# Kernel tuning notes

Measured on AMD Instinct MI355X. Metric: run time of the kernel, lower is better.

Reference implementation:

```python
import jax, jax.numpy as jnp
import numpy as np

N, H, C, G = 50000, 16, 8, 128   # nodes, heads, per-head channels, graphs
F_IN, NUM_CLASSES = 128, 2
E = 800000
HC = H * C
NEG_SLOPE = 0.2
BN_EPS = 1e-5


def setup_inputs() -> dict:
    key = jax.random.key(0)
    ks = jax.random.split(key, 32)
    s = 0.1
    p = lambda k, shape: (jax.random.normal(k, shape, jnp.float32) * s)
    inp = {
        "x": jax.random.normal(ks[0], (N, F_IN), jnp.float32),
        "edge_index": jax.random.randint(ks[1], (2, E), 0, N, dtype=jnp.int32),
        "batch": jnp.sort(jax.random.randint(ks[2], (N,), 0, G, dtype=jnp.int32)),
        # GAT layer 1 (in=F_IN)
        "W1": p(ks[3], (F_IN, HC)), "b1": p(ks[4], (HC,)),
        "asrc1": p(ks[5], (H, C)), "adst1": p(ks[6], (H, C)),
        "g1": 1.0 + p(ks[7], (HC,)), "beta1": p(ks[8], (HC,)),
        # GAT layer 2 (in=HC)
        "W2": p(ks[9], (HC, HC)), "b2": p(ks[10], (HC,)),
        "asrc2": p(ks[11], (H, C)), "adst2": p(ks[12], (H, C)),
        "g2": 1.0 + p(ks[13], (HC,)), "beta2": p(ks[14], (HC,)),
        # GAT layer 3
        "W3": p(ks[15], (HC, HC)), "b3": p(ks[16], (HC,)),
        "asrc3": p(ks[17], (H, C)), "adst3": p(ks[18], (H, C)),
        "g3": 1.0 + p(ks[19], (HC,)), "beta3": p(ks[20], (HC,)),
        # final linear + bn4
        "Wl": p(ks[21], (2 * HC, NUM_CLASSES)), "bl": p(ks[22], (NUM_CLASSES,)),
        "g4": 1.0 + p(ks[23], (NUM_CLASSES,)), "beta4": p(ks[24], (NUM_CLASSES,)),
    }
    return inp


def _gat(x, src, dst, W, b, asrc, adst):
    # x: [N, F_in] -> h: [N, H, C]
    h = (x @ W).reshape(N, H, C)
    a_s = jnp.einsum("nhc,hc->nh", h, asrc)  # [N,H]
    a_d = jnp.einsum("nhc,hc->nh", h, adst)
    e = jax.nn.leaky_relu(a_s[src] + a_d[dst], NEG_SLOPE)  # [E',H]
    # per-destination softmax (every node has a self loop -> segments non-empty)
    e_max = jax.ops.segment_max(e, dst, num_segments=N)
    ex = jnp.exp(e - e_max[dst])
    denom = jax.ops.segment_sum(ex, dst, num_segments=N)
    alpha = ex / (denom[dst] + 1e-16)  # [E',H]
    out = jax.ops.segment_sum(h[src] * alpha[:, :, None], dst, num_segments=N)
    return out.reshape(N, HC) + b


def _bn(x, g, beta):
    mu = jnp.mean(x, axis=0)
    var = jnp.mean((x - mu) ** 2, axis=0)  # biased, training-mode BN
    return (x - mu) * jax.lax.rsqrt(var + BN_EPS) * g + beta


def reference(x, edge_index, batch,
              W1, b1, asrc1, adst1, g1, beta1,
              W2, b2, asrc2, adst2, g2, beta2,
              W3, b3, asrc3, adst3, g3, beta3,
              Wl, bl, g4, beta4):
    # add self loops once (add_self_loops=True in every GATConv)
    loop = jnp.arange(N, dtype=edge_index.dtype)
    src = jnp.concatenate([edge_index[0], loop])
    dst = jnp.concatenate([edge_index[1], loop])

    h = jax.nn.relu(_bn(_gat(x, src, dst, W1, b1, asrc1, adst1), g1, beta1))
    h = jax.nn.relu(_bn(_gat(h, src, dst, W2, b2, asrc2, adst2), g2, beta2))
    h = jax.nn.relu(_bn(_gat(h, src, dst, W3, b3, asrc3, adst3), g3, beta3))

    pooled_sum = jax.ops.segment_sum(h, batch, num_segments=G)        # [G,HC]
    cnt = jax.ops.segment_sum(jnp.ones((N,), h.dtype), batch, num_segments=G)
    pooled_mean = pooled_sum / jnp.maximum(cnt, 1.0)[:, None]
    z = jnp.concatenate([pooled_mean, pooled_sum], axis=1)            # [G,2*HC]
    z = z @ Wl + bl
    return _bn(z, g4, beta4)
```

## Files before the change

### kernel.cpp

```cpp
#include <hip/hip_runtime.h>

#define NN 50000
#define NHEADS 16
#define NGRAPH 128
#define NEDGE 800000
#define NEP (NEDGE + NN)

#define EPB 2048
#define NBLK 416
#define NBUK 391
#define CASTB 3125
#define WTB 192

typedef float4 f4;
typedef __attribute__((ext_vector_type(4))) float f32x4;
typedef __attribute__((ext_vector_type(8))) short s8;

__device__ inline unsigned short f2b(float f) {
  union { float f; unsigned u; } v; v.f = f;
  unsigned r = v.u + 0x7FFFu + ((v.u >> 16) & 1u);
  return (unsigned short)(r >> 16);
}
__device__ inline float b2f(unsigned u16) {
  union { unsigned u; float f; } v; v.u = u16 << 16;
  return v.f;
}
__device__ inline float blo(unsigned u) {
  union { unsigned u; float f; } v; v.u = u << 16;
  return v.f;
}
__device__ inline float bhi(unsigned u) {
  union { unsigned u; float f; } v; v.u = u & 0xffff0000u;
  return v.f;
}


__global__ __launch_bounds__(256) void k_bhist(const int* __restrict__ ei, int* __restrict__ cntmat) {
  __shared__ int hist[NBUK];
  int t = threadIdx.x, b = blockIdx.x;
  for (int k = t; k < NBUK; k += 256) hist[k] = 0;
  __syncthreads();
  int i0 = b * EPB;
  int i1 = i0 + EPB < NEP ? i0 + EPB : NEP;
  for (int i = i0 + t; i < i1; i += 256) {
    int d = (i < NEDGE) ? ei[NEDGE + i] : (i - NEDGE);
    atomicAdd(&hist[d >> 7], 1);
  }
  __syncthreads();
  for (int k = t; k < NBUK; k += 256) cntmat[b * NBUK + k] = hist[k];
}

__global__ __launch_bounds__(512) void k_bscan(int* __restrict__ cntmat, int* __restrict__ btotal) {
  __shared__ int buf[512];
  int t = threadIdx.x, k = blockIdx.x;
  int v = (t < NBLK) ? cntmat[t * NBUK + k] : 0;
  buf[t] = v;
  __syncthreads();
  for (int off = 1; off < 512; off <<= 1) {
    int y = (t >= off) ? buf[t - off] : 0;
    __syncthreads();
    buf[t] += y;
    __syncthreads();
  }
  if (t < NBLK) cntmat[t * NBUK + k] = buf[t] - v;
  if (t == 511) btotal[k] = buf[511];
}

__global__ __launch_bounds__(512) void k_bbase(const int* __restrict__ btotal, int* __restrict__ bbase) {
  __shared__ int buf[512];
  int t = threadIdx.x;
  int v = (t < NBUK) ? btotal[t] : 0;
  buf[t] = v;
  __syncthreads();
  for (int off = 1; off < 512; off <<= 1) {
    int y = (t >= off) ? buf[t - off] : 0;
    __syncthreads();
    buf[t] += y;
    __syncthreads();
  }
  if (t < NBUK) bbase[t] = buf[t] - v;
  if (t == 511) bbase[NBUK] = buf[511];
}

__global__ __launch_bounds__(256) void k_bscatter(const int* __restrict__ ei, const int* __restrict__ cntmat,
                                                  const int* __restrict__ bbase, unsigned* __restrict__ pairs) {
  __shared__ int cur[NBUK];
  int t = threadIdx.x, b = blockIdx.x;
  for (int k = t; k < NBUK; k += 256) cur[k] = bbase[k] + cntmat[b * NBUK + k];
  __syncthreads();
  int i0 = b * EPB;
  int i1 = i0 + EPB < NEP ? i0 + EPB : NEP;
  for (int i = i0 + t; i < i1; i += 256) {
    int s, d;
    if (i < NEDGE) { s = ei[i]; d = ei[NEDGE + i]; }
    else { s = d = i - NEDGE; }
    int pos = atomicAdd(&cur[d >> 7], 1);
    pairs[pos] = ((unsigned)(d & 127) << 16) | (unsigned)s;
  }
}

__global__ __launch_bounds__(256) void k_bfinal(const unsigned* __restrict__ pairs, const int* __restrict__ bbase,
                                                int* __restrict__ row_off, int* __restrict__ colp) {
  __shared__ int cnt[128];
  __shared__ int buf[128];
  __shared__ int cur[128];
  int t = threadIdx.x, k = blockIdx.x;
  int n0 = k << 7;
  if (t < 128) cnt[t] = 0;
  __syncthreads();
  int p0 = bbase[k], p1 = bbase[k + 1];
  for (int i = p0 + t; i < p1; i += 256) atomicAdd(&cnt[pairs[i] >> 16], 1);
  __syncthreads();
  if (t < 128) buf[t] = cnt[t];
  __syncthreads();
  for (int off = 1; off < 128; off <<= 1) {
    int y = (t < 128 && t >= off) ? buf[t - off] : 0;
    __syncthreads();
    if (t < 128) buf[t] += y;
    __syncthreads();
  }
  if (t < 128) {
    int excl = buf[t] - cnt[t];
    cur[t] = p0 + excl;
    if (n0 + t < NN) row_off[n0 + t] = p0 + excl;
  }
  if (k == NBUK - 1 && t == 0) row_off[NN] = p1;
  __syncthreads();
  for (int i = p0 + t; i < p1; i += 256) {
    unsigned r = pairs[i];
    int pos = atomicAdd(&cur[r >> 16], 1);
    colp[pos] = (int)(r & 0xffffu);
  }
}


__global__ __launch_bounds__(256) void k_prep(const float* __restrict__ X, unsigned short* __restrict__ Xb,
                                              const float* __restrict__ W0, const float* __restrict__ W1, const float* __restrict__ W2,
                                              unsigned short* __restrict__ T0, unsigned short* __restrict__ T1, unsigned short* __restrict__ T2,
                                              const int* __restrict__ batch, int* __restrict__ gstart) {
  int b = blockIdx.x, t = threadIdx.x;
  if (b < CASTB) {
    int i = b * 256 + t;
    const f4* X4 = (const f4*)X;
    f4 a = X4[2 * i], c = X4[2 * i + 1];
    uint4 o;
    o.x = (unsigned)f2b(a.x) | ((unsigned)f2b(a.y) << 16);
    o.y = (unsigned)f2b(a.z) | ((unsigned)f2b(a.w) << 16);
    o.z = (unsigned)f2b(c.x) | ((unsigned)f2b(c.y) << 16);
    o.w = (unsigned)f2b(c.z) | ((unsigned)f2b(c.w) << 16);
    ((uint4*)Xb)[i] = o;
  } else if (b < CASTB + WTB) {
    int idx = (b - CASTB) * 256 + t;
    int L = idx >> 14, r = idx & 16383;
    int n = r >> 7, kk = r & 127;
    const float* W = (L == 0) ? W0 : (L == 1) ? W1 : W2;
    unsigned short* T = (L == 0) ? T0 : (L == 1) ? T1 : T2;
    T[n * 128 + kk] = f2b(W[kk * 128 + n]);
  } else {
    int g = t;
    if (g > NGRAPH) return;
    int lo = 0, hi = NN;
    while (lo < hi) { int mid = (lo + hi) >> 1; if (batch[mid] < g) lo = mid + 1; else hi = mid; }
    gstart[g] = lo;
  }
}


template<int FUSE>
__global__ __launch_bounds__(256) void k_gemm_t(const unsigned short* __restrict__ A, const unsigned short* __restrict__ Wt,
                                                const float* __restrict__ sc, unsigned short* __restrict__ Hb) {
  int w = threadIdx.x >> 6, l = threadIdx.x & 63;
  int r0 = blockIdx.x * 128 + w * 32;
  int lr = l & 15, lg = l >> 4;
  f32x4 acc[2][8];
#pragma unroll
  for (int m = 0; m < 2; ++m)
#pragma unroll
    for (int n = 0; n < 8; ++n) acc[m][n] = (f32x4){0.f, 0.f, 0.f, 0.f};

#pragma unroll
  for (int ks = 0; ks < 4; ++ks) {
    int koff = ks * 32 + lg * 8;
    s8 a[2];
    if constexpr (FUSE) {
      f4 s0 = *(const f4*)(sc + koff),       s1 = *(const f4*)(sc + koff + 4);
      f4 h0 = *(const f4*)(sc + 128 + koff), h1 = *(const f4*)(sc + 128 + koff + 4);
#pragma unroll
      for (int m = 0; m < 2; ++m) {
        int row = r0 + m * 16 + lr;
        row = (row < NN) ? row : (NN - 1);
        uint4 raw = *(const uint4*)(A + (size_t)row * 128 + koff);
        float v0 = fmaxf(blo(raw.x) * s0.x + h0.x, 0.f);
        float v1 = fmaxf(bhi(raw.x) * s0.y + h0.y, 0.f);
        float v2 = fmaxf(blo(raw.y) * s0.z + h0.z, 0.f);
        float v3 = fmaxf(bhi(raw.y) * s0.w + h0.w, 0.f);
        float v4 = fmaxf(blo(raw.z) * s1.x + h1.x, 0.f);
        float v5 = fmaxf(bhi(raw.z) * s1.y + h1.y, 0.f);
        float v6 = fmaxf(blo(raw.w) * s1.z + h1.z, 0.f);
        float v7 = fmaxf(bhi(raw.w) * s1.w + h1.w, 0.f);
        union { s8 v; uint4 u; } pk;
        pk.u.x = (unsigned)f2b(v0) | ((unsigned)f2b(v1) << 16);
        pk.u.y = (unsigned)f2b(v2) | ((unsigned)f2b(v3) << 16);
        pk.u.z = (unsigned)f2b(v4) | ((unsigned)f2b(v5) << 16);
        pk.u.w = (unsigned)f2b(v6) | ((unsigned)f2b(v7) << 16);
        a[m] = pk.v;
      }
    } else {
#pragma unroll
      for (int m = 0; m < 2; ++m) {
        int row = r0 + m * 16 + lr;
        row = (row < NN) ? row : (NN - 1);
        a[m] = *(const s8*)(A + (size_t)row * 128 + koff);
      }
    }
    s8 b[8];
#pragma unroll
    for (int n = 0; n < 8; ++n)
      b[n] = *(const s8*)(Wt + (size_t)(n * 16 + lr) * 128 + koff);
#pragma unroll
    for (int m = 0; m < 2; ++m)
#pragma unroll
      for (int n = 0; n < 8; ++n)
        acc[m][n] = __builtin_amdgcn_mfma_f32_16x16x32_bf16(a[m], b[n], acc[m][n], 0, 0, 0);
  }

#pragma unroll
  for (int m = 0; m < 2; ++m) {
    int rowb = r0 + m * 16 + lg * 4;
#pragma unroll
    for (int n = 0; n < 8; ++n) {
      int colb = n * 16 + lr;
#pragma unroll
      for (int reg = 0; reg < 4; ++reg) {
        int row = rowb + reg;
        if (row < NN) Hb[(size_t)row * 128 + colb] = f2b(acc[m][n][reg]);
      }
    }
  }
}


__global__ __launch_bounds__(256) void k_coef(const unsigned short* __restrict__ Hb, const float* __restrict__ asrc,
                                              const float* __restrict__ adst, unsigned short* __restrict__ Asb, float* __restrict__ Ad) {
  int idx = blockIdx.x * 256 + threadIdx.x;
  if (idx >= NN * NHEADS) return;
  int n = idx >> 4, hd = idx & 15;
  uint4 hv = *(const uint4*)(Hb + (size_t)n * 128 + hd * 8);
  float h0 = blo(hv.x), h1 = bhi(hv.x);
  float h2 = blo(hv.y), h3 = bhi(hv.y);
  float h4 = blo(hv.z), h5 = bhi(hv.z);
  float h6 = blo(hv.w), h7 = bhi(hv.w);
  const f4* s4 = (const f4*)(asrc + hd * 8);
  const f4* d4 = (const f4*)(adst + hd * 8);
  f4 sa = s4[0], sb = s4[1], da = d4[0], db = d4[1];
  float as_v = h0 * sa.x + h1 * sa.y + h2 * sa.z + h3 * sa.w + h4 * sb.x + h5 * sb.y + h6 * sb.z + h7 * sb.w;
  float ad_v = h0 * da.x + h1 * da.y + h2 * da.z + h3 * da.w + h4 * db.x + h5 * db.y + h6 * db.z + h7 * db.w;
  Asb[idx] = f2b(as_v);
  Ad[idx] = ad_v;
}


__global__ __launch_bounds__(256, 4) void k_agg(const unsigned short* __restrict__ Hb, const unsigned short* __restrict__ Asb,
                                                const float* __restrict__ Ad,
                                                const int* __restrict__ row_off, const int* __restrict__ col,
                                                unsigned short* __restrict__ Vb) {
  int node = blockIdx.x * 8 + (threadIdx.x >> 5);
  int l = threadIdx.x & 31;
  int h = l & 15, par = l >> 4;
  int e0 = row_off[node], e1 = row_off[node + 1];
  float adh = Ad[node * 16 + h];
  float den = 0.f;
  float acc[8] = {0.f, 0.f, 0.f, 0.f, 0.f, 0.f, 0.f, 0.f};
  int j = e0 + par;
  for (; j + 14 < e1; j += 16) {
    int s[8];
#pragma unroll
    for (int q = 0; q < 8; ++q) s[q] = col[j + 2 * q];
    float a[8];
#pragma unroll
    for (int q = 0; q < 8; ++q) a[q] = b2f(Asb[s[q] * 16 + h]);
    uint4 p[8];
#pragma unroll
    for (int q = 0; q < 8; ++q) p[q] = *(const uint4*)(Hb + (size_t)s[q] * 128 + h * 8);
#pragma unroll
    for (int q = 0; q < 8; ++q) {
      float e = a[q] + adh;
      e = (e > 0.f) ? e : 0.2f * e;
      a[q] = __expf(e);
      den += a[q];
    }
#pragma unroll
    for (int q = 0; q < 8; ++q) {
      acc[0] += a[q] * blo(p[q].x); acc[1] += a[q] * bhi(p[q].x);
      acc[2] += a[q] * blo(p[q].y); acc[3] += a[q] * bhi(p[q].y);
      acc[4] += a[q] * blo(p[q].z); acc[5] += a[q] * bhi(p[q].z);
      acc[6] += a[q] * blo(p[q].w); acc[7] += a[q] * bhi(p[q].w);
    }
  }
  for (; j + 6 < e1; j += 8) {
    int s[4];
#pragma unroll
    for (int q = 0; q < 4; ++q) s[q] = col[j + 2 * q];
    float a[4];
#pragma unroll
    for (int q = 0; q < 4; ++q) a[q] = b2f(Asb[s[q] * 16 + h]);
    uint4 p[4];
#pragma unroll
    for (int q = 0; q < 4; ++q) p[q] = *(const uint4*)(Hb + (size_t)s[q] * 128 + h * 8);
#pragma unroll
    for (int q = 0; q < 4; ++q) {
      float e = a[q] + adh;
      e = (e > 0.f) ? e : 0.2f * e;
      a[q] = __expf(e);
      den += a[q];
    }
#pragma unroll
    for (int q = 0; q < 4; ++q) {
      acc[0] += a[q] * blo(p[q].x); acc[1] += a[q] * bhi(p[q].x);
      acc[2] += a[q] * blo(p[q].y); acc[3] += a[q] * bhi(p[q].y);
      acc[4] += a[q] * blo(p[q].z); acc[5] += a[q] * bhi(p[q].z);
      acc[6] += a[q] * blo(p[q].w); acc[7] += a[q] * bhi(p[q].w);
    }
  }
  for (; j < e1; j += 2) {
    int s0 = col[j];
    float a0 = b2f(Asb[s0 * 16 + h]) + adh;
    uint4 p0 = *(const uint4*)(Hb + (size_t)s0 * 128 + h * 8);
    a0 = (a0 > 0.f) ? a0 : 0.2f * a0;
    float x0 = __expf(a0);
    den += x0;
    acc[0] += x0 * blo(p0.x); acc[1] += x0 * bhi(p0.x);
    acc[2] += x0 * blo(p0.y); acc[3] += x0 * bhi(p0.y);
    acc[4] += x0 * blo(p0.z); acc[5] += x0 * bhi(p0.z);
    acc[6] += x0 * blo(p0.w); acc[7] += x0 * bhi(p0.w);
  }
  den += __shfl_xor(den, 16);
#pragma unroll
  for (int k = 0; k < 8; ++k) acc[k] += __shfl_xor(acc[k], 16);
  if (par == 0) {
    float inv = 1.f / (den + 1e-16f);
    uint4 o;
    o.x = (unsigned)f2b(acc[0] * inv) | ((unsigned)f2b(acc[1] * inv) << 16);
    o.y = (unsigned)f2b(acc[2] * inv) | ((unsigned)f2b(acc[3] * inv) << 16);
    o.z = (unsigned)f2b(acc[4] * inv) | ((unsigned)f2b(acc[5] * inv) << 16);
    o.w = (unsigned)f2b(acc[6] * inv) | ((unsigned)f2b(acc[7] * inv) << 16);
    *(uint4*)(Vb + (size_t)node * 128 + h * 8) = o;
  }
}


#define BN_CHUNK 391

__global__ __launch_bounds__(256) void k_bnreduce(const unsigned short* __restrict__ Vb, float* __restrict__ partS, float* __restrict__ partQ) {
  int t = threadIdx.x;
  int c4 = t & 31, rs = t >> 5;
  int r0 = blockIdx.x * BN_CHUNK + rs;
  int rend = blockIdx.x * BN_CHUNK + BN_CHUNK;
  if (rend > NN) rend = NN;
  float s0 = 0.f, s1 = 0.f, s2 = 0.f, s3 = 0.f;
  float q0 = 0.f, q1 = 0.f, q2 = 0.f, q3 = 0.f;
  for (int r = r0; r < rend; r += 8) {
    uint2 p = *(const uint2*)(Vb + (size_t)r * 128 + c4 * 4);
    float v0 = blo(p.x), v1 = bhi(p.x);
    float v2 = blo(p.y), v3 = bhi(p.y);
    s0 += v0; s1 += v1; s2 += v2; s3 += v3;
    q0 += v0 * v0; q1 += v1 * v1; q2 += v2 * v2; q3 += v3 * v3;
  }
  __shared__ float sm[8][32][8];
  sm[rs][c4][0] = s0; sm[rs][c4][1] = s1; sm[rs][c4][2] = s2; sm[rs][c4][3] = s3;
  sm[rs][c4][4] = q0; sm[rs][c4][5] = q1; sm[rs][c4][6] = q2; sm[rs][c4][7] = q3;
  __syncthreads();
  if (t < 32) {
#pragma unroll
    for (int k = 0; k < 4; ++k) {
      float S = 0.f, Q = 0.f;
#pragma unroll
      for (int r = 0; r < 8; ++r) { S += sm[r][t][k]; Q += sm[r][t][4 + k]; }
      partS[blockIdx.x * 128 + t * 4 + k] = S;
      partQ[blockIdx.x * 128 + t * 4 + k] = Q;
    }
  }
}

__global__ __launch_bounds__(512) void k_bnfin(const float* __restrict__ partS, const float* __restrict__ partQ,
                                               const float* __restrict__ gam, const float* __restrict__ bet,
                                               float* __restrict__ sc) {
  int t = threadIdx.x;
  int c = t & 127, q = (t >> 7) & 1, hf = t >> 8;
  const float* src = q ? partQ : partS;
  float s = 0.f;
#pragma unroll 8
  for (int i = hf * 64; i < hf * 64 + 64; ++i) s += src[i * 128 + c];
  __shared__ float sm[512];
  sm[t] = s;
  __syncthreads();
  if (t < 128) {
    float S = sm[t] + sm[t + 256];
    float Q = sm[t + 128] + sm[t + 384];
    float mean = S * (1.f / NN);
    float var = fmaxf(Q * (1.f / NN) - mean * mean, 0.f);
    float sg = gam[t] * rsqrtf(var + 1e-5f);
    sc[t] = sg;
    sc[128 + t] = bet[t] - mean * sg;
  }
}


__global__ __launch_bounds__(256) void k_pool(const unsigned short* __restrict__ Vb, const float* __restrict__ sc,
                                              const int* __restrict__ gstart, float* __restrict__ pooled) {
  int g = blockIdx.x >> 2, chunk = blockIdx.x & 3;
  int t = threadIdx.x;
  int c4 = t & 31, rs = t >> 5;
  f4 s = ((const f4*)sc)[c4], sh = ((const f4*)sc)[32 + c4];
  int r0 = gstart[g], r1 = gstart[g + 1];
  float s0 = 0.f, s1 = 0.f, s2 = 0.f, s3 = 0.f;
  for (int r = r0 + chunk + 4 * rs; r < r1; r += 32) {
    uint2 p = *(const uint2*)(Vb + (size_t)r * 128 + c4 * 4);
    s0 += fmaxf(blo(p.x) * s.x + sh.x, 0.f);
    s1 += fmaxf(bhi(p.x) * s.y + sh.y, 0.f);
    s2 += fmaxf(blo(p.y) * s.z + sh.z, 0.f);
    s3 += fmaxf(bhi(p.y) * s.w + sh.w, 0.f);
  }
  __shared__ float sm[8][32][4];
  sm[rs][c4][0] = s0; sm[rs][c4][1] = s1; sm[rs][c4][2] = s2; sm[rs][c4][3] = s3;
  __syncthreads();
  if (t < 32) {
#pragma unroll
    for (int k = 0; k < 4; ++k) {
      float S = 0.f;
#pragma unroll
      for (int r = 0; r < 8; ++r) S += sm[r][t][k];
      atomicAdd(&pooled[g * 128 + t * 4 + k], S);
    }
  }
}

__global__ __launch_bounds__(256) void k_final(const float* __restrict__ pooled, const int* __restrict__ gstart,
                                               const float* __restrict__ Wl, const float* __restrict__ bl,
                                               const float* __restrict__ g4, const float* __restrict__ b4,
                                               float* __restrict__ out) {
  int t = threadIdx.x;
  int g = t >> 1, cls = t & 1;
  float cnt = fmaxf((float)(gstart[g + 1] - gstart[g]), 1.f);
  float inv = 1.f / cnt;
  float z = bl[cls];
  for (int f = 0; f < 128; ++f) {
    float ps = pooled[g * 128 + f];
    z += ps * inv * Wl[f * 2 + cls] + ps * Wl[(128 + f) * 2 + cls];
  }
  __shared__ float zs[256];
  __shared__ float st[4];
  zs[t] = z;
  __syncthreads();
  if (t < 2) {
    float s = 0.f, s2 = 0.f;
    for (int gg = 0; gg < 128; ++gg) { float v = zs[gg * 2 + t]; s += v; s2 += v * v; }
    float mean = s * (1.f / 128.f);
    float var = s2 * (1.f / 128.f) - mean * mean;
    var = fmaxf(var, 0.f);
    float sc = g4[t] * rsqrtf(var + 1e-5f);
    st[t] = sc; st[2 + t] = b4[t] - mean * sc;
  }
  __syncthreads();
  out[t] = zs[t] * st[cls] + st[2 + cls];
}


extern "C" void kernel_launch(void* const* d_in, const int* in_sizes, int n_in,
                              void* d_out, int out_size, void* d_ws, size_t ws_size,
                              hipStream_t stream) {
  const float* x     = (const float*)d_in[0];
  const int*   ei    = (const int*)d_in[1];
  const int*   batch = (const int*)d_in[2];
  const float* W[3]    = {(const float*)d_in[3],  (const float*)d_in[9],  (const float*)d_in[15]};
  const float* asrc[3] = {(const float*)d_in[5],  (const float*)d_in[11], (const float*)d_in[17]};
  const float* adst[3] = {(const float*)d_in[6],  (const float*)d_in[12], (const float*)d_in[18]};
  const float* gam[3]  = {(const float*)d_in[7],  (const float*)d_in[13], (const float*)d_in[19]};
  const float* bet[3]  = {(const float*)d_in[8],  (const float*)d_in[14], (const float*)d_in[20]};
  const float* Wl    = (const float*)d_in[21];
  const float* bl    = (const float*)d_in[22];
  const float* g4    = (const float*)d_in[23];
  const float* beta4 = (const float*)d_in[24];

  char* ws = (char*)d_ws;
  size_t off = 0;
  auto alloc = [&](size_t bytes) -> void* {
    void* p = (void*)(ws + off);
    off += (bytes + 255) & ~(size_t)255;
    return p;
  };

  int* row_off  = (int*)alloc((size_t)(NN + 1) * 4);
  int* col      = (int*)alloc((size_t)NEP * 4);
  int* cntmat   = (int*)alloc((size_t)NBLK * NBUK * 4);
  int* btotal   = (int*)alloc((size_t)NBUK * 4);
  int* bbase    = (int*)alloc((size_t)(NBUK + 1) * 4);
  unsigned* pairs = (unsigned*)alloc((size_t)NEP * 4);
  unsigned short* Xb = (unsigned short*)alloc((size_t)NN * 128 * 2);
  unsigned short* Hb = (unsigned short*)alloc((size_t)NN * 128 * 2);
  unsigned short* Vb = (unsigned short*)alloc((size_t)NN * 128 * 2);
  unsigned short* Asb = (unsigned short*)alloc((size_t)NN * 16 * 2);
  float* Ad     = (float*)alloc((size_t)NN * 16 * 4);
  unsigned short* Wt0 = (unsigned short*)alloc(16384 * 2);
  unsigned short* Wt1 = (unsigned short*)alloc(16384 * 2);
  unsigned short* Wt2 = (unsigned short*)alloc(16384 * 2);
  const unsigned short* Wt[3] = {Wt0, Wt1, Wt2};
  float* partS  = (float*)alloc(128 * 128 * 4);
  float* partQ  = (float*)alloc(128 * 128 * 4);
  float* bn_sc  = (float*)alloc(256 * 4);
  float* pooled = (float*)alloc((size_t)NGRAPH * 128 * 4);
  int* gstart   = (int*)alloc((size_t)(NGRAPH + 1) * 4);

  k_bhist<<<NBLK, 256, 0, stream>>>(ei, cntmat);
  k_bscan<<<NBUK, 512, 0, stream>>>(cntmat, btotal);
  k_bbase<<<1, 512, 0, stream>>>(btotal, bbase);
  k_bscatter<<<NBLK, 256, 0, stream>>>(ei, cntmat, bbase, pairs);
  k_bfinal<<<NBUK, 256, 0, stream>>>(pairs, bbase, row_off, col);

  k_prep<<<CASTB + WTB + 1, 256, 0, stream>>>(x, Xb, W[0], W[1], W[2], Wt0, Wt1, Wt2, batch, gstart);

  hipMemsetAsync(pooled, 0, (size_t)NGRAPH * 128 * 4, stream);

  for (int L = 0; L < 3; ++L) {
    if (L == 0)
      k_gemm_t<0><<<(NN + 127) / 128, 256, 0, stream>>>(Xb, Wt[L], nullptr, Hb);
    else
      k_gemm_t<1><<<(NN + 127) / 128, 256, 0, stream>>>(Vb, Wt[L], bn_sc, Hb);
    k_coef<<<(NN * 16) / 256, 256, 0, stream>>>(Hb, asrc[L], adst[L], Asb, Ad);
    k_agg<<<NN / 8, 256, 0, stream>>>(Hb, Asb, Ad, row_off, col, Vb);
    k_bnreduce<<<128, 256, 0, stream>>>(Vb, partS, partQ);
    k_bnfin<<<1, 512, 0, stream>>>(partS, partQ, gam[L], bet[L], bn_sc);
  }

  k_pool<<<NGRAPH * 4, 256, 0, stream>>>(Vb, bn_sc, gstart, pooled);
  k_final<<<1, 256, 0, stream>>>(pooled, gstart, Wl, bl, g4, beta4, (float*)d_out);
}
```

Baseline: 291.2 us.

## Fold attention coefficients into GEMM, one lane group per node, drop pool atomics

```diff
diff --git a/kernel.cpp b/kernel.cpp
--- a/kernel.cpp
+++ b/kernel.cpp
@@ -11,6 +11,7 @@
 #define NBUK 391
 #define CASTB 3125
 #define WTB 192
+#define WASB 48
 
 typedef float4 f4;
 typedef __attribute__((ext_vector_type(4))) float f32x4;
@@ -136,6 +137,8 @@
 
 __global__ __launch_bounds__(256) void k_prep(const float* __restrict__ X, unsigned short* __restrict__ Xb,
                                               const float* __restrict__ W0, const float* __restrict__ W1, const float* __restrict__ W2,
+                                              const float* __restrict__ as0, const float* __restrict__ as1, const float* __restrict__ as2,
+                                              const float* __restrict__ ad0, const float* __restrict__ ad1, const float* __restrict__ ad2,
                                               unsigned short* __restrict__ T0, unsigned short* __restrict__ T1, unsigned short* __restrict__ T2,
                                               const int* __restrict__ batch, int* __restrict__ gstart) {
   int b = blockIdx.x, t = threadIdx.x;
@@ -156,6 +159,19 @@
     const float* W = (L == 0) ? W0 : (L == 1) ? W1 : W2;
     unsigned short* T = (L == 0) ? T0 : (L == 1) ? T1 : T2;
     T[n * 128 + kk] = f2b(W[kk * 128 + n]);
+  } else if (b < CASTB + WTB + WASB) {
+    int idx = (b - CASTB - WTB) * 256 + t;
+    int L = idx >> 12, r = idx & 4095;
+    int h2 = r >> 7, kk = r & 127;
+    int h = h2 & 15;
+    const float* W = (L == 0) ? W0 : (L == 1) ? W1 : W2;
+    const float* av = (h2 < 16) ? ((L == 0) ? as0 : (L == 1) ? as1 : as2)
+                                : ((L == 0) ? ad0 : (L == 1) ? ad1 : ad2);
+    unsigned short* T = (L == 0) ? T0 : (L == 1) ? T1 : T2;
+    float s = 0.f;
+#pragma unroll
+    for (int c = 0; c < 8; ++c) s += W[kk * 128 + h * 8 + c] * av[h * 8 + c];
+    T[(128 + h2) * 128 + kk] = f2b(s);
   } else {
     int g = t;
     if (g > NGRAPH) return;
@@ -168,15 +184,16 @@
 
 template<int FUSE>
 __global__ __launch_bounds__(256) void k_gemm_t(const unsigned short* __restrict__ A, const unsigned short* __restrict__ Wt,
-                                                const float* __restrict__ sc, unsigned short* __restrict__ Hb) {
+                                                const float* __restrict__ sc, unsigned short* __restrict__ Hb,
+                                                unsigned short* __restrict__ Asb, float* __restrict__ Ad) {
   int w = threadIdx.x >> 6, l = threadIdx.x & 63;
   int r0 = blockIdx.x * 128 + w * 32;
   int lr = l & 15, lg = l >> 4;
-  f32x4 acc[2][8];
+  f32x4 acc[2][10];
 #pragma unroll
   for (int m = 0; m < 2; ++m)
 #pragma unroll
-    for (int n = 0; n < 8; ++n) acc[m][n] = (f32x4){0.f, 0.f, 0.f, 0.f};
+    for (int n = 0; n < 10; ++n) acc[m][n] = (f32x4){0.f, 0.f, 0.f, 0.f};
 
 #pragma unroll
   for (int ks = 0; ks < 4; ++ks) {
@@ -213,15 +230,13 @@
         a[m] = *(const s8*)(A + (size_t)row * 128 + koff);
       }
     }
-    s8 b[8];
-#pragma unroll
-    for (int n = 0; n < 8; ++n)
-      b[n] = *(const s8*)(Wt + (size_t)(n * 16 + lr) * 128 + koff);
-#pragma unroll
-    for (int m = 0; m < 2; ++m)
-#pragma unroll
-      for (int n = 0; n < 8; ++n)
-        acc[m][n] = __builtin_amdgcn_mfma_f32_16x16x32_bf16(a[m], b[n], acc[m][n], 0, 0, 0);
+#pragma unroll
+    for (int n = 0; n < 10; ++n) {
+      s8 b = *(const s8*)(Wt + (size_t)(n * 16 + lr) * 128 + koff);
+#pragma unroll
+      for (int m = 0; m < 2; ++m)
+        acc[m][n] = __builtin_amdgcn_mfma_f32_16x16x32_bf16(a[m], b, acc[m][n], 0, 0, 0);
+    }
   }
 
 #pragma unroll
@@ -236,27 +251,15 @@
         if (row < NN) Hb[(size_t)row * 128 + colb] = f2b(acc[m][n][reg]);
       }
     }
-  }
-}
-
-
-__global__ __launch_bounds__(256) void k_coef(const unsigned short* __restrict__ Hb, const float* __restrict__ asrc,
-                                              const float* __restrict__ adst, unsigned short* __restrict__ Asb, float* __restrict__ Ad) {
-  int idx = blockIdx.x * 256 + threadIdx.x;
-  if (idx >= NN * NHEADS) return;
-  int n = idx >> 4, hd = idx & 15;
-  uint4 hv = *(const uint4*)(Hb + (size_t)n * 128 + hd * 8);
-  float h0 = blo(hv.x), h1 = bhi(hv.x);
-  float h2 = blo(hv.y), h3 = bhi(hv.y);
-  float h4 = blo(hv.z), h5 = bhi(hv.z);
-  float h6 = blo(hv.w), h7 = bhi(hv.w);
-  const f4* s4 = (const f4*)(asrc + hd * 8);
-  const f4* d4 = (const f4*)(adst + hd * 8);
-  f4 sa = s4[0], sb = s4[1], da = d4[0], db = d4[1];
-  float as_v = h0 * sa.x + h1 * sa.y + h2 * sa.z + h3 * sa.w + h4 * sb.x + h5 * sb.y + h6 * sb.z + h7 * sb.w;
-  float ad_v = h0 * da.x + h1 * da.y + h2 * da.z + h3 * da.w + h4 * db.x + h5 * db.y + h6 * db.z + h7 * db.w;
-  Asb[idx] = f2b(as_v);
-  Ad[idx] = ad_v;
+#pragma unroll
+    for (int reg = 0; reg < 4; ++reg) {
+      int row = rowb + reg;
+      if (row < NN) {
+        Asb[row * 16 + lr] = f2b(acc[m][8][reg]);
+        Ad[row * 16 + lr] = acc[m][9][reg];
+      }
+    }
+  }
 }
 
 
@@ -264,18 +267,17 @@
                                                 const float* __restrict__ Ad,
                                                 const int* __restrict__ row_off, const int* __restrict__ col,
                                                 unsigned short* __restrict__ Vb) {
-  int node = blockIdx.x * 8 + (threadIdx.x >> 5);
-  int l = threadIdx.x & 31;
-  int h = l & 15, par = l >> 4;
+  int node = blockIdx.x * 16 + (threadIdx.x >> 4);
+  int h = threadIdx.x & 15;
   int e0 = row_off[node], e1 = row_off[node + 1];
   float adh = Ad[node * 16 + h];
   float den = 0.f;
   float acc[8] = {0.f, 0.f, 0.f, 0.f, 0.f, 0.f, 0.f, 0.f};
-  int j = e0 + par;
-  for (; j + 14 < e1; j += 16) {
+  int j = e0;
+  for (; j + 7 < e1; j += 8) {
     int s[8];
 #pragma unroll
-    for (int q = 0; q < 8; ++q) s[q] = col[j + 2 * q];
+    for (int q = 0; q < 8; ++q) s[q] = col[j + q];
     float a[8];
 #pragma unroll
     for (int q = 0; q < 8; ++q) a[q] = b2f(Asb[s[q] * 16 + h]);
@@ -297,10 +299,10 @@
       acc[6] += a[q] * blo(p[q].w); acc[7] += a[q] * bhi(p[q].w);
     }
   }
-  for (; j + 6 < e1; j += 8) {
+  for (; j + 3 < e1; j += 4) {
     int s[4];
 #pragma unroll
-    for (int q = 0; q < 4; ++q) s[q] = col[j + 2 * q];
+    for (int q = 0; q < 4; ++q) s[q] = col[j + q];
     float a[4];
 #pragma unroll
     for (int q = 0; q < 4; ++q) a[q] = b2f(Asb[s[q] * 16 + h]);
@@ -322,7 +324,7 @@
       acc[6] += a[q] * blo(p[q].w); acc[7] += a[q] * bhi(p[q].w);
     }
   }
-  for (; j < e1; j += 2) {
+  for (; j < e1; ++j) {
     int s0 = col[j];
     float a0 = b2f(Asb[s0 * 16 + h]) + adh;
     uint4 p0 = *(const uint4*)(Hb + (size_t)s0 * 128 + h * 8);
@@ -334,18 +336,13 @@
     acc[4] += x0 * blo(p0.z); acc[5] += x0 * bhi(p0.z);
     acc[6] += x0 * blo(p0.w); acc[7] += x0 * bhi(p0.w);
   }
-  den += __shfl_xor(den, 16);
-#pragma unroll
-  for (int k = 0; k < 8; ++k) acc[k] += __shfl_xor(acc[k], 16);
-  if (par == 0) {
-    float inv = 1.f / (den + 1e-16f);
-    uint4 o;
-    o.x = (unsigned)f2b(acc[0] * inv) | ((unsigned)f2b(acc[1] * inv) << 16);
-    o.y = (unsigned)f2b(acc[2] * inv) | ((unsigned)f2b(acc[3] * inv) << 16);
-    o.z = (unsigned)f2b(acc[4] * inv) | ((unsigned)f2b(acc[5] * inv) << 16);
-    o.w = (unsigned)f2b(acc[6] * inv) | ((unsigned)f2b(acc[7] * inv) << 16);
-    *(uint4*)(Vb + (size_t)node * 128 + h * 8) = o;
-  }
+  float inv = 1.f / (den + 1e-16f);
+  uint4 o;
+  o.x = (unsigned)f2b(acc[0] * inv) | ((unsigned)f2b(acc[1] * inv) << 16);
+  o.y = (unsigned)f2b(acc[2] * inv) | ((unsigned)f2b(acc[3] * inv) << 16);
+  o.z = (unsigned)f2b(acc[4] * inv) | ((unsigned)f2b(acc[5] * inv) << 16);
+  o.w = (unsigned)f2b(acc[6] * inv) | ((unsigned)f2b(acc[7] * inv) << 16);
+  *(uint4*)(Vb + (size_t)node * 128 + h * 8) = o;
 }
 
 
@@ -407,7 +404,7 @@
 
 
 __global__ __launch_bounds__(256) void k_pool(const unsigned short* __restrict__ Vb, const float* __restrict__ sc,
-                                              const int* __restrict__ gstart, float* __restrict__ pooled) {
+                                              const int* __restrict__ gstart, float* __restrict__ pp) {
   int g = blockIdx.x >> 2, chunk = blockIdx.x & 3;
   int t = threadIdx.x;
   int c4 = t & 31, rs = t >> 5;
@@ -430,12 +427,12 @@
       float S = 0.f;
 #pragma unroll
       for (int r = 0; r < 8; ++r) S += sm[r][t][k];
-      atomicAdd(&pooled[g * 128 + t * 4 + k], S);
-    }
-  }
-}
-
-__global__ __launch_bounds__(256) void k_final(const float* __restrict__ pooled, const int* __restrict__ gstart,
+      pp[(size_t)blockIdx.x * 128 + t * 4 + k] = S;
+    }
+  }
+}
+
+__global__ __launch_bounds__(256) void k_final(const float* __restrict__ pp, const int* __restrict__ gstart,
                                                const float* __restrict__ Wl, const float* __restrict__ bl,
                                                const float* __restrict__ g4, const float* __restrict__ b4,
                                                float* __restrict__ out) {
@@ -445,7 +442,8 @@
   float inv = 1.f / cnt;
   float z = bl[cls];
   for (int f = 0; f < 128; ++f) {
-    float ps = pooled[g * 128 + f];
+    float ps = pp[(size_t)(g * 4 + 0) * 128 + f] + pp[(size_t)(g * 4 + 1) * 128 + f]
+             + pp[(size_t)(g * 4 + 2) * 128 + f] + pp[(size_t)(g * 4 + 3) * 128 + f];
     z += ps * inv * Wl[f * 2 + cls] + ps * Wl[(128 + f) * 2 + cls];
   }
   __shared__ float zs[256];
@@ -501,14 +499,14 @@
   unsigned short* Vb = (unsigned short*)alloc((size_t)NN * 128 * 2);
   unsigned short* Asb = (unsigned short*)alloc((size_t)NN * 16 * 2);
   float* Ad     = (float*)alloc((size_t)NN * 16 * 4);
-  unsigned short* Wt0 = (unsigned short*)alloc(16384 * 2);
-  unsigned short* Wt1 = (unsigned short*)alloc(16384 * 2);
-  unsigned short* Wt2 = (unsigned short*)alloc(16384 * 2);
+  unsigned short* Wt0 = (unsigned short*)alloc((size_t)160 * 128 * 2);
+  unsigned short* Wt1 = (unsigned short*)alloc((size_t)160 * 128 * 2);
+  unsigned short* Wt2 = (unsigned short*)alloc((size_t)160 * 128 * 2);
   const unsigned short* Wt[3] = {Wt0, Wt1, Wt2};
   float* partS  = (float*)alloc(128 * 128 * 4);
   float* partQ  = (float*)alloc(128 * 128 * 4);
   float* bn_sc  = (float*)alloc(256 * 4);
-  float* pooled = (float*)alloc((size_t)NGRAPH * 128 * 4);
+  float* pp     = (float*)alloc((size_t)NGRAPH * 4 * 128 * 4);
   int* gstart   = (int*)alloc((size_t)(NGRAPH + 1) * 4);
 
   k_bhist<<<NBLK, 256, 0, stream>>>(ei, cntmat);
@@ -517,21 +515,20 @@
   k_bscatter<<<NBLK, 256, 0, stream>>>(ei, cntmat, bbase, pairs);
   k_bfinal<<<NBUK, 256, 0, stream>>>(pairs, bbase, row_off, col);
 
-  k_prep<<<CASTB + WTB + 1, 256, 0, stream>>>(x, Xb, W[0], W[1], W[2], Wt0, Wt1, Wt2, batch, gstart);
-
-  hipMemsetAsync(pooled, 0, (size_t)NGRAPH * 128 * 4, stream);
+  k_prep<<<CASTB + WTB + WASB + 1, 256, 0, stream>>>(x, Xb, W[0], W[1], W[2],
+                                                     asrc[0], asrc[1], asrc[2], adst[0], adst[1], adst[2],
+                                                     Wt0, Wt1, Wt2, batch, gstart);
 
   for (int L = 0; L < 3; ++L) {
     if (L == 0)
-      k_gemm_t<0><<<(NN + 127) / 128, 256, 0, stream>>>(Xb, Wt[L], nullptr, Hb);
+      k_gemm_t<0><<<(NN + 127) / 128, 256, 0, stream>>>(Xb, Wt[L], nullptr, Hb, Asb, Ad);
     else
-      k_gemm_t<1><<<(NN + 127) / 128, 256, 0, stream>>>(Vb, Wt[L], bn_sc, Hb);
-    k_coef<<<(NN * 16) / 256, 256, 0, stream>>>(Hb, asrc[L], adst[L], Asb, Ad);
-    k_agg<<<NN / 8, 256, 0, stream>>>(Hb, Asb, Ad, row_off, col, Vb);
+      k_gemm_t<1><<<(NN + 127) / 128, 256, 0, stream>>>(Vb, Wt[L], bn_sc, Hb, Asb, Ad);
+    k_agg<<<NN / 16, 256, 0, stream>>>(Hb, Asb, Ad, row_off, col, Vb);
     k_bnreduce<<<128, 256, 0, stream>>>(Vb, partS, partQ);
     k_bnfin<<<1, 512, 0, stream>>>(partS, partQ, gam[L], bet[L], bn_sc);
   }
 
-  k_pool<<<NGRAPH * 4, 256, 0, stream>>>(Vb, bn_sc, gstart, pooled);
-  k_final<<<1, 256, 0, stream>>>(pooled, gstart, Wl, bl, g4, beta4, (float*)d_out);
-}
+  k_pool<<<NGRAPH * 4, 256, 0, stream>>>(Vb, bn_sc, gstart, pp);
+  k_final<<<1, 256, 0, stream>>>(pp, gstart, Wl, bl, g4, beta4, (float*)d_out);
+}
```

Result: slower. 297.4 us (+2.1%).
